# Kernel optimization log

Measured on AMD Instinct MI355X. Metric: run time of the kernel, lower is better.

Reference implementation:

```python
import jax, jax.numpy as jnp
import numpy as np

EMB = 1024
NEG_INF = float(-2**32 + 1)
EPS_SCALE = 1e-8   # epsilon added to sqrt(scale) in attention_dot
LN_EPS = 1e-5      # torch.nn.LayerNorm default eps


def _layernorm(x, w, b):
    mu = jnp.mean(x, axis=-1, keepdims=True)
    var = jnp.mean(jnp.square(x - mu), axis=-1, keepdims=True)
    return (x - mu) * jax.lax.rsqrt(var + LN_EPS) * w + b


def setup_inputs() -> dict:
    key = jax.random.key(0)
    ks = jax.random.split(key, 6)
    B, Lq, Lk, E = 8, 2048, 2048, EMB
    queries = jax.random.normal(ks[0], (B, Lq, E), dtype=jnp.float32)
    keys = jax.random.normal(ks[1], (B, Lk, E), dtype=jnp.float32)
    query_masks = jnp.ones((B, Lq), dtype=jnp.float32)
    key_masks = jnp.ones((B, Lk), dtype=jnp.float32)
    # xavier_uniform for Linear(E, E): limit = sqrt(6/(E+E))
    lim = float(np.sqrt(6.0 / (E + E)))
    W1 = jax.random.uniform(ks[2], (E, E), minval=-lim, maxval=lim, dtype=jnp.float32)
    b1 = jnp.zeros((E,), dtype=jnp.float32)
    W2 = jax.random.uniform(ks[3], (E, E), minval=-lim, maxval=lim, dtype=jnp.float32)
    b2 = jnp.zeros((E,), dtype=jnp.float32)
    ln_w = jnp.ones((E,), dtype=jnp.float32)
    ln_b = jnp.zeros((E,), dtype=jnp.float32)
    ln2_w = jnp.ones((E,), dtype=jnp.float32)
    ln2_b = jnp.zeros((E,), dtype=jnp.float32)
    return {"queries": queries, "keys": keys, "query_masks": query_masks,
            "key_masks": key_masks, "ln_w": ln_w, "ln_b": ln_b,
            "ln2_w": ln2_w, "ln2_b": ln2_b, "W1": W1, "b1": b1,
            "W2": W2, "b2": b2}


def reference(queries, keys, query_masks, key_masks, ln_w, ln_b, ln2_w, ln2_b, W1, b1, W2, b2):
    E = queries.shape[-1]
    # scores [B, Lq, Lk]
    sim = jnp.einsum('bik,bjk->bij', queries, keys)
    sim = sim / (jnp.sqrt(jnp.float32(max(1.0, E))) + EPS_SCALE)
    # key mask applied pre-softmax
    sim = jnp.where(key_masks[:, None, :] == 0, jnp.float32(NEG_INF), sim)
    sim = jax.nn.softmax(sim, axis=-1)
    # query mask applied post-softmax
    sim = sim * query_masks[:, :, None]
    attn_out = jnp.einsum('bij,bjk->bik', sim, keys)
    # residual + LayerNorm
    x = _layernorm(attn_out + queries, ln_w, ln_b)
    # FFN: Linear -> ReLU -> Linear, residual, LayerNorm
    h = jax.nn.relu(x @ W1.T + b1)
    y = h @ W2.T + b2
    return _layernorm(y + x, ln2_w, ln2_b)
```

## Files before the change

### kernel.cpp

```cpp
#include <hip/hip_runtime.h>
#include <hip/hip_bf16.h>
#include <stdint.h>

#define NB    8
#define LQ    2048
#define LKK   2048
#define EMBD  1024

typedef __bf16 bf16_t;
typedef __bf16 bf16x8 __attribute__((ext_vector_type(8)));
typedef __bf16 bf16x4 __attribute__((ext_vector_type(4)));
typedef float  f32x4  __attribute__((ext_vector_type(4)));

__device__ __forceinline__ bf16_t f2bf(float x) {
  union { float f; uint32_t u; } v; v.f = x;
  uint32_t r = v.u + 0x7fffu + ((v.u >> 16) & 1u);
  uint16_t h = (uint16_t)(r >> 16);
  return __builtin_bit_cast(bf16_t, h);
}

__device__ __forceinline__ float wred_sum(float v) {
#pragma unroll
  for (int o = 32; o; o >>= 1) v += __shfl_xor(v, o);
  return v;
}
__device__ __forceinline__ float wred_max(float v) {
#pragma unroll
  for (int o = 32; o; o >>= 1) v = fmaxf(v, __shfl_xor(v, o));
  return v;
}

template<int EPI>
__global__ __launch_bounds__(512, 1)
void gemm_nt(const bf16_t* __restrict__ A, const bf16_t* __restrict__ B,
             float* __restrict__ Cf, bf16_t* __restrict__ Cb,
             const float* __restrict__ bias, float scale,
             int M, int N, int K, long sA, long sB, long sC)
{
  __shared__ __align__(16) char smem[131072];
  typedef bf16_t ldsbuf_t[8][256][8];
  ldsbuf_t* Abuf = (ldsbuf_t*)smem;
  ldsbuf_t* Bbuf = (ldsbuf_t*)(smem + 65536);

  const int tid  = threadIdx.x;
  const int lane = tid & 63;
  const int wave = tid >> 6;
  const int wq   = wave & 3;
  const int bz   = blockIdx.z;

  const bf16_t* Ab = A + (long)bz * sA;
  const bf16_t* Bb = B + (long)bz * sB;

  const int bm = blockIdx.x * 256;
  const int bn = blockIdx.y * 256;
  const int wm = (wave >> 2) * 128;

  f32x4 acc[8][4] = {};

  const int srow = tid & 255;
  const int sslc = tid >> 8;

  const int fr = lane & 15;
  const int fs = lane >> 4;

  auto STAGE = [&](int bufi, int kt) {
#pragma unroll
    for (int i = 0; i < 4; i++) {
      const int slc = sslc + 2 * i;
      __builtin_amdgcn_global_load_lds(
        (const __attribute__((address_space(1))) void*)(Ab + (long)(bm + srow) * K + kt + slc * 8),
        (__attribute__((address_space(3))) void*)((char*)&Abuf[bufi][0][0][0] + (tid + i * 512) * 16),
        16, 0, 0);
    }
#pragma unroll
    for (int i = 0; i < 4; i++) {
      const int slc = sslc + 2 * i;
      __builtin_amdgcn_global_load_lds(
        (const __attribute__((address_space(1))) void*)(Bb + (long)(bn + srow) * K + kt + slc * 8),
        (__attribute__((address_space(3))) void*)((char*)&Bbuf[bufi][0][0][0] + (tid + i * 512) * 16),
        16, 0, 0);
    }
  };

  auto COMPUTE = [&](int bufi) {
#pragma unroll
    for (int kk = 0; kk < 2; kk++) {
      bf16x8 af[8], bfg[4];
#pragma unroll
      for (int m = 0; m < 8; m++)
        af[m] = *(const bf16x8*)&Abuf[bufi][4 * kk + fs][wm + m * 16 + fr][0];
#pragma unroll
      for (int n = 0; n < 4; n++)
        bfg[n] = *(const bf16x8*)&Bbuf[bufi][4 * kk + fs][n * 64 + wq * 16 + fr][0];
#pragma unroll
      for (int m = 0; m < 8; m++)
#pragma unroll
        for (int n = 0; n < 4; n++)
          acc[m][n] = __builtin_amdgcn_mfma_f32_16x16x32_bf16(af[m], bfg[n], acc[m][n], 0, 0, 0);
    }
  };

  STAGE(0, 0);
  __syncthreads();
  int buf = 0;
  for (int kt = 64; kt < K; kt += 64) {
    STAGE(buf ^ 1, kt);
    COMPUTE(buf);
    __syncthreads();
    buf ^= 1;
  }
  COMPUTE(buf);

  float* slab = (float*)smem;
  const long cbase = (long)bz * sC;
#pragma unroll
  for (int h = 0; h < 2; h++) {
    __syncthreads();
#pragma unroll
    for (int nn = 0; nn < 2; nn++) {
      const int n = 2 * h + nn;
      const int colb = nn * 64 + wq * 16 + fr;
#pragma unroll
      for (int m = 0; m < 8; m++) {
        const int rbase = wm + m * 16 + ((lane >> 4) << 2);
#pragma unroll
        for (int j = 0; j < 4; j++) {
          const int row = rbase + j;
          slab[row * 128 + (colb ^ (((row >> 2) & 1) << 4))] = acc[m][n][j];
        }
      }
    }
    __syncthreads();
    const int hcol = bn + h * 128;
    if constexpr (EPI == 3) {
#pragma unroll
      for (int p = 0; p < 16; p++) {
        const int row = p * 16 + (tid >> 5);
        const int c4  = (tid & 31) * 4;
        f32x4 v = *(const f32x4*)&slab[row * 128 + (c4 ^ (((row >> 2) & 1) << 4))];
        const float4 bv = *(const float4*)&bias[hcol + c4];
        v[0] += bv.x; v[1] += bv.y; v[2] += bv.z; v[3] += bv.w;
        *(f32x4*)&Cf[cbase + (long)(bm + row) * N + hcol + c4] = v;
      }
    } else {
#pragma unroll
      for (int p = 0; p < 8; p++) {
        const int row  = p * 32 + (tid >> 4);
        const int c8   = (tid & 15) * 8;
        const int flip = ((row >> 2) & 1) << 4;
        const f32x4 v0 = *(const f32x4*)&slab[row * 128 + (c8 ^ flip)];
        const f32x4 v1 = *(const f32x4*)&slab[row * 128 + ((c8 + 4) ^ flip)];
        const float vv[8] = {v0[0], v0[1], v0[2], v0[3], v1[0], v1[1], v1[2], v1[3]};
        bf16x8 o;
        if constexpr (EPI == 0) {
#pragma unroll
          for (int e = 0; e < 8; e++) o[e] = f2bf(vv[e] * scale);
        } else if constexpr (EPI == 1) {
#pragma unroll
          for (int e = 0; e < 8; e++) o[e] = f2bf(vv[e]);
        } else {
          const float4 b0 = *(const float4*)&bias[hcol + c8];
          const float4 b1 = *(const float4*)&bias[hcol + c8 + 4];
          const float bb[8] = {b0.x, b0.y, b0.z, b0.w, b1.x, b1.y, b1.z, b1.w};
#pragma unroll
          for (int e = 0; e < 8; e++) o[e] = f2bf(fmaxf(vv[e] + bb[e], 0.0f));
        }
        *(bf16x8*)&Cb[cbase + (long)(bm + row) * N + hcol + c8] = o;
      }
    }
  }
}

__global__ __launch_bounds__(256)
void softmax_kernel(const bf16_t* __restrict__ S, bf16_t* __restrict__ P,
                    const float* __restrict__ km, const float* __restrict__ qm)
{
  __shared__ float red[8];
  const int r = blockIdx.x;
  const int b = r >> 11;
  const int t = threadIdx.x;
  const bf16_t* row = S + (long)r * LKK;

  const bf16x8 sv = *(const bf16x8*)(row + t * 8);
  const float4 k0 = ((const float4*)(km + (long)b * LKK))[2 * t];
  const float4 k1 = ((const float4*)(km + (long)b * LKK))[2 * t + 1];
  const float kmv[8] = {k0.x, k0.y, k0.z, k0.w, k1.x, k1.y, k1.z, k1.w};

  float v[8];
  float mx = -3.4e38f;
#pragma unroll
  for (int i = 0; i < 8; i++) {
    float s = (float)sv[i];
    s = (kmv[i] == 0.0f) ? -4294967295.0f : s;
    v[i] = s;
    mx = fmaxf(mx, s);
  }
  mx = wred_max(mx);
  if ((t & 63) == 0) red[t >> 6] = mx;
  __syncthreads();
  mx = fmaxf(fmaxf(red[0], red[1]), fmaxf(red[2], red[3]));

  float sum = 0.0f;
#pragma unroll
  for (int i = 0; i < 8; i++) {
    const float e = __expf(v[i] - mx);
    v[i] = e;
    sum += e;
  }
  sum = wred_sum(sum);
  if ((t & 63) == 0) red[4 + (t >> 6)] = sum;
  __syncthreads();
  sum = red[4] + red[5] + red[6] + red[7];

  const float rs = qm[r] / sum;
  bf16x8 o;
#pragma unroll
  for (int i = 0; i < 8; i++) o[i] = f2bf(v[i] * rs);
  *(bf16x8*)(P + (long)r * LKK + t * 8) = o;
}

template<int MODE>
__global__ __launch_bounds__(256)
void ln_kernel(const void* __restrict__ Xv, const void* __restrict__ Rv,
               const float* __restrict__ w, const float* __restrict__ bp,
               void* __restrict__ Yv)
{
  __shared__ float red[8];
  const long r = blockIdx.x;
  const int t = threadIdx.x;

  float x0, x1, x2, x3;
  if constexpr (MODE & 1) {
    const bf16x4 xv = ((const bf16x4*)((const bf16_t*)Xv + r * EMBD))[t];
    x0 = (float)xv[0]; x1 = (float)xv[1]; x2 = (float)xv[2]; x3 = (float)xv[3];
  } else {
    const float4 xv = ((const float4*)((const float*)Xv + r * EMBD))[t];
    x0 = xv.x; x1 = xv.y; x2 = xv.z; x3 = xv.w;
  }
  float r0, r1, r2, r3;
  if constexpr (MODE & 2) {
    const bf16x4 rv = ((const bf16x4*)((const bf16_t*)Rv + r * EMBD))[t];
    r0 = (float)rv[0]; r1 = (float)rv[1]; r2 = (float)rv[2]; r3 = (float)rv[3];
  } else {
    const float4 rv = ((const float4*)((const float*)Rv + r * EMBD))[t];
    r0 = rv.x; r1 = rv.y; r2 = rv.z; r3 = rv.w;
  }
  const float s0 = x0 + r0, s1 = x1 + r1, s2 = x2 + r2, s3 = x3 + r3;

  float sum = wred_sum(s0 + s1 + s2 + s3);
  if ((t & 63) == 0) red[t >> 6] = sum;
  __syncthreads();
  const float mu = (red[0] + red[1] + red[2] + red[3]) * (1.0f / EMBD);

  const float d0 = s0 - mu, d1 = s1 - mu, d2 = s2 - mu, d3 = s3 - mu;
  float sq = wred_sum(d0 * d0 + d1 * d1 + d2 * d2 + d3 * d3);
  if ((t & 63) == 0) red[4 + (t >> 6)] = sq;
  __syncthreads();
  const float var = (red[4] + red[5] + red[6] + red[7]) * (1.0f / EMBD);
  const float rstd = rsqrtf(var + 1e-5f);

  const float4 wv = ((const float4*)w)[t];
  const float4 bv = ((const float4*)bp)[t];
  const float y0 = d0 * rstd * wv.x + bv.x;
  const float y1 = d1 * rstd * wv.y + bv.y;
  const float y2 = d2 * rstd * wv.z + bv.z;
  const float y3 = d3 * rstd * wv.w + bv.w;

  if constexpr (MODE & 4) {
    bf16x4 o; o[0] = f2bf(y0); o[1] = f2bf(y1); o[2] = f2bf(y2); o[3] = f2bf(y3);
    ((bf16x4*)((bf16_t*)Yv + r * EMBD))[t] = o;
  } else {
    ((float4*)((float*)Yv + r * EMBD))[t] = make_float4(y0, y1, y2, y3);
  }
}

__global__ void cvt_kernel(const float* __restrict__ in, bf16_t* __restrict__ out, long n4)
{
  long i = (long)blockIdx.x * 256 + threadIdx.x;
  const long stride = (long)gridDim.x * 256;
  for (; i < n4; i += stride) {
    const float4 v = ((const float4*)in)[i];
    bf16x4 o; o[0] = f2bf(v.x); o[1] = f2bf(v.y); o[2] = f2bf(v.z); o[3] = f2bf(v.w);
    ((bf16x4*)out)[i] = o;
  }
}

__global__ __launch_bounds__(256)
void transpose_cvt(const float* __restrict__ in, bf16_t* __restrict__ outT,
                   bf16_t* __restrict__ outS, int rows, int cols)
{
  __shared__ bf16_t tile[32][33];
  const long zb = (long)blockIdx.z * rows * cols;
  const int cb = blockIdx.x * 32;
  const int rb = blockIdx.y * 32;
  const int tx = threadIdx.x & 31;
  const int ty = threadIdx.x >> 5;
#pragma unroll
  for (int i = 0; i < 4; i++) {
    const int rr = ty + i * 8;
    const bf16_t v = f2bf(in[zb + (long)(rb + rr) * cols + cb + tx]);
    tile[rr][tx] = v;
    if (outS != nullptr) outS[zb + (long)(rb + rr) * cols + cb + tx] = v;
  }
  __syncthreads();
#pragma unroll
  for (int i = 0; i < 4; i++) {
    const int cc = ty + i * 8;
    outT[zb + (long)(cb + cc) * rows + rb + tx] = tile[tx][cc];
  }
}

extern "C" void kernel_launch(void* const* d_in, const int* in_sizes, int n_in,
                              void* d_out, int out_size, void* d_ws, size_t ws_size,
                              hipStream_t stream)
{
  const float* q    = (const float*)d_in[0];
  const float* k    = (const float*)d_in[1];
  const float* qm   = (const float*)d_in[2];
  const float* km   = (const float*)d_in[3];
  const float* lnw  = (const float*)d_in[4];
  const float* lnb  = (const float*)d_in[5];
  const float* ln2w = (const float*)d_in[6];
  const float* ln2b = (const float*)d_in[7];
  const float* W1   = (const float*)d_in[8];
  const float* b1   = (const float*)d_in[9];
  const float* W2   = (const float*)d_in[10];
  const float* b2   = (const float*)d_in[11];

  char* ws = (char*)d_ws;
  char* ob = (char*)d_out;
  const float scale = 0.03125f;
  const long MB = 1L << 20;
  const long QE = (long)LQ * EMBD;
  const long SS = (long)LQ * LKK;

  if (ws_size >= 100 * MB) {
    bf16_t* Qb   = (bf16_t*)ws;
    bf16_t* attn = (bf16_t*)ws;
    bf16_t* Kb   = (bf16_t*)(ws + 32 * MB);
    bf16_t* h    = (bf16_t*)(ws + 32 * MB);
    bf16_t* Kt   = (bf16_t*)(ws + 64 * MB);
    bf16_t* W1b  = (bf16_t*)(ws + 96 * MB);
    bf16_t* W2b  = (bf16_t*)(ws + 98 * MB);
    bf16_t* Sb   = (bf16_t*)ob;
    float*  y    = (float*)ob;

    cvt_kernel<<<1024, 256, 0, stream>>>(W1, W1b, (long)EMBD * EMBD / 4);
    cvt_kernel<<<1024, 256, 0, stream>>>(W2, W2b, (long)EMBD * EMBD / 4);
    cvt_kernel<<<4096, 256, 0, stream>>>(q, Qb, (long)NB * QE / 4);
    transpose_cvt<<<dim3(EMBD / 32, LKK / 32, NB), 256, 0, stream>>>(k, Kt, Kb, LKK, EMBD);

    gemm_nt<0><<<dim3(LQ / 256, LKK / 256, NB), 512, 0, stream>>>(
        Qb, Kb, nullptr, Sb, nullptr, scale, LQ, LKK, EMBD, QE, QE, SS);
    softmax_kernel<<<NB * LQ, 256, 0, stream>>>(Sb, Sb, km, qm);
    gemm_nt<1><<<dim3(LQ / 256, EMBD / 256, NB), 512, 0, stream>>>(
        Sb, Kt, nullptr, attn, nullptr, 0.0f, LQ, EMBD, LKK, SS, (long)EMBD * LKK, QE);
    ln_kernel<5><<<NB * LQ, 256, 0, stream>>>(attn, q, lnw, lnb, attn);
    gemm_nt<2><<<dim3(NB * LQ / 256, EMBD / 256, 1), 512, 0, stream>>>(
        attn, W1b, nullptr, h, b1, 0.0f, NB * LQ, EMBD, EMBD, 0, 0, 0);
    gemm_nt<3><<<dim3(NB * LQ / 256, EMBD / 256, 1), 512, 0, stream>>>(
        h, W2b, y, nullptr, b2, 0.0f, NB * LQ, EMBD, EMBD, 0, 0, 0);
    ln_kernel<2><<<NB * LQ, 256, 0, stream>>>(y, attn, ln2w, ln2b, y);

  } else if (ws_size >= 52 * MB) {
    bf16_t* attn = (bf16_t*)ws;
    bf16_t* W1b  = (bf16_t*)(ws + 32 * MB);
    bf16_t* W2b  = (bf16_t*)(ws + 34 * MB);
    bf16_t* Kth  = (bf16_t*)(ws + 36 * MB);
    bf16_t* h    = (bf16_t*)(ws + 36 * MB);
    bf16_t* Sb   = (bf16_t*)ob;
    bf16_t* Qbh  = (bf16_t*)(ob + 32 * MB);
    bf16_t* Kbh  = (bf16_t*)(ob + 48 * MB);
    float*  y    = (float*)ob;

    cvt_kernel<<<1024, 256, 0, stream>>>(W1, W1b, (long)EMBD * EMBD / 4);
    cvt_kernel<<<1024, 256, 0, stream>>>(W2, W2b, (long)EMBD * EMBD / 4);

    for (int it = 0; it < 2; it++) {
      const int bo = it * 4;
      const float* qh = q + bo * QE;
      const float* kh = k + bo * QE;
      cvt_kernel<<<2048, 256, 0, stream>>>(qh, Qbh, 4 * QE / 4);
      transpose_cvt<<<dim3(EMBD / 32, LKK / 32, 4), 256, 0, stream>>>(kh, Kth, Kbh, LKK, EMBD);

      gemm_nt<0><<<dim3(LQ / 256, LKK / 256, 4), 512, 0, stream>>>(
          Qbh, Kbh, nullptr, Sb, nullptr, scale, LQ, LKK, EMBD, QE, QE, SS);
      softmax_kernel<<<4 * LQ, 256, 0, stream>>>(Sb, Sb, km + bo * LKK, qm + bo * LQ);
      gemm_nt<1><<<dim3(LQ / 256, EMBD / 256, 4), 512, 0, stream>>>(
          Sb, Kth, nullptr, attn + bo * QE, nullptr, 0.0f, LQ, EMBD, LKK,
          SS, (long)EMBD * LKK, QE);
    }
    ln_kernel<5><<<NB * LQ, 256, 0, stream>>>(attn, q, lnw, lnb, attn);
    for (int c = 0; c < 2; c++) {
      bf16_t* xc = attn + (long)c * 8192 * EMBD;
      float*  yc = y + (long)c * 8192 * EMBD;
      gemm_nt<2><<<dim3(8192 / 256, EMBD / 256, 1), 512, 0, stream>>>(
          xc, W1b, nullptr, h, b1, 0.0f, 8192, EMBD, EMBD, 0, 0, 0);
      gemm_nt<3><<<dim3(8192 / 256, EMBD / 256, 1), 512, 0, stream>>>(
          h, W2b, yc, nullptr, b2, 0.0f, 8192, EMBD, EMBD, 0, 0, 0);
    }
    ln_kernel<2><<<NB * LQ, 256, 0, stream>>>(y, attn, ln2w, ln2b, y);

  } else {
    if (ws_size < 44 * MB) return;
    bf16_t* attn = (bf16_t*)ws;
    bf16_t* W1b  = (bf16_t*)(ws + 32 * MB);
    bf16_t* W2b  = (bf16_t*)(ws + 34 * MB);
    bf16_t* h    = (bf16_t*)(ws + 36 * MB);
    bf16_t* Sb   = (bf16_t*)(ob);
    bf16_t* Pb   = (bf16_t*)(ob + 8 * MB);
    bf16_t* Qbb  = (bf16_t*)(ob + 16 * MB);
    bf16_t* Kbb  = (bf16_t*)(ob + 20 * MB);
    bf16_t* Ktb  = (bf16_t*)(ob + 24 * MB);

    cvt_kernel<<<1024, 256, 0, stream>>>(W1, W1b, (long)EMBD * EMBD / 4);
    cvt_kernel<<<1024, 256, 0, stream>>>(W2, W2b, (long)EMBD * EMBD / 4);

    for (int b = 0; b < NB; b++) {
      const float* qb = q + b * QE;
      const float* kb = k + b * QE;
      cvt_kernel<<<2048, 256, 0, stream>>>(qb, Qbb, QE / 4);
      transpose_cvt<<<dim3(EMBD / 32, LKK / 32, 1), 256, 0, stream>>>(kb, Ktb, Kbb, LKK, EMBD);

      gemm_nt<0><<<dim3(LQ / 256, LKK / 256, 1), 512, 0, stream>>>(
          Qbb, Kbb, nullptr, Sb, nullptr, scale, LQ, LKK, EMBD, 0, 0, 0);
      softmax_kernel<<<LQ, 256, 0, stream>>>(Sb, Pb, km + (long)b * LKK, qm + (long)b * LQ);
      gemm_nt<1><<<dim3(LQ / 256, EMBD / 256, 1), 512, 0, stream>>>(
          Pb, Ktb, nullptr, attn + b * QE, nullptr, 0.0f, LQ, EMBD, LKK, 0, 0, 0);
    }
    ln_kernel<5><<<NB * LQ, 256, 0, stream>>>(attn, q, lnw, lnb, attn);
    for (int c = 0; c < 4; c++) {
      bf16_t* xc = attn + (long)c * 4096 * EMBD;
      float*  yc = (float*)d_out + (long)c * 4096 * EMBD;
      gemm_nt<2><<<dim3(4096 / 256, EMBD / 256, 1), 512, 0, stream>>>(
          xc, W1b, nullptr, h, b1, 0.0f, 4096, EMBD, EMBD, 0, 0, 0);
      gemm_nt<3><<<dim3(4096 / 256, EMBD / 256, 1), 512, 0, stream>>>(
          h, W2b, yc, nullptr, b2, 0.0f, 4096, EMBD, EMBD, 0, 0, 0);
      ln_kernel<2><<<4096, 256, 0, stream>>>(yc, xc, ln2w, ln2b, yc);
    }
  }
}
```

Baseline: 456.0 us.

## Add 32-wide K GEMM variant with 64KB LDS for two blocks per CU

Adds gemm_nt32, which stages K in steps of 32 instead of 64, halving LDS to 64KB and declaring launch bounds of two blocks per CU. The intent is higher occupancy, so one block's memory stalls can overlap with another's MFMA work. The epilogue is factored out and now writes the slab in four 64-column passes with a new XOR swizzle, so it fits in the smaller LDS. The QK, PV and first FFN GEMMs switch to the new kernel. The risks are twice as many barriers per K, and register pressure from the 128-float accumulator when capped for two blocks, which could cause spills.

```diff
diff --git a/kernel.cpp b/kernel.cpp
--- a/kernel.cpp
+++ b/kernel.cpp
@@ -28,6 +28,72 @@
 #pragma unroll
   for (int o = 32; o; o >>= 1) v = fmaxf(v, __shfl_xor(v, o));
   return v;
+}
+
+__device__ __forceinline__ int slab_flip(int row) {
+  return ((row ^ (row >> 2)) & 3) << 4;
+}
+
+template<int EPI>
+__device__ __forceinline__ void gemm_epilogue(
+    f32x4 (&acc)[8][4], char* smem, float* Cf, bf16_t* Cb,
+    const float* bias, float scale, int N, long cbase,
+    int bm, int bn, int wm, int wq, int tid, int lane)
+{
+  float* slab = (float*)smem;
+  const int fr = lane & 15;
+  const int g4 = (lane >> 4) << 2;
+#pragma unroll
+  for (int n = 0; n < 4; n++) {
+    __syncthreads();
+#pragma unroll
+    for (int m = 0; m < 8; m++) {
+      const int rbase = wm + m * 16 + g4;
+#pragma unroll
+      for (int j = 0; j < 4; j++) {
+        const int row = rbase + j;
+        slab[row * 64 + ((wq * 16 + fr) ^ slab_flip(row))] = acc[m][n][j];
+      }
+    }
+    __syncthreads();
+    const int ncol = bn + n * 64;
+    if constexpr (EPI == 3) {
+#pragma unroll
+      for (int p = 0; p < 8; p++) {
+        const int row = p * 32 + (tid >> 4);
+        const int c4  = (tid & 15) * 4;
+        f32x4 v = *(const f32x4*)&slab[row * 64 + (c4 ^ slab_flip(row))];
+        const float4 bv = *(const float4*)&bias[ncol + c4];
+        v[0] += bv.x; v[1] += bv.y; v[2] += bv.z; v[3] += bv.w;
+        *(f32x4*)&Cf[cbase + (long)(bm + row) * N + ncol + c4] = v;
+      }
+    } else {
+#pragma unroll
+      for (int p = 0; p < 4; p++) {
+        const int row  = p * 64 + (tid >> 3);
+        const int c8   = (tid & 7) * 8;
+        const int flip = slab_flip(row);
+        const f32x4 v0 = *(const f32x4*)&slab[row * 64 + (c8 ^ flip)];
+        const f32x4 v1 = *(const f32x4*)&slab[row * 64 + ((c8 + 4) ^ flip)];
+        const float vv[8] = {v0[0], v0[1], v0[2], v0[3], v1[0], v1[1], v1[2], v1[3]};
+        bf16x8 o;
+        if constexpr (EPI == 0) {
+#pragma unroll
+          for (int e = 0; e < 8; e++) o[e] = f2bf(vv[e] * scale);
+        } else if constexpr (EPI == 1) {
+#pragma unroll
+          for (int e = 0; e < 8; e++) o[e] = f2bf(vv[e]);
+        } else {
+          const float4 b0 = *(const float4*)&bias[ncol + c8];
+          const float4 b1 = *(const float4*)&bias[ncol + c8 + 4];
+          const float bb[8] = {b0.x, b0.y, b0.z, b0.w, b1.x, b1.y, b1.z, b1.w};
+#pragma unroll
+          for (int e = 0; e < 8; e++) o[e] = f2bf(fmaxf(vv[e] + bb[e], 0.0f));
+        }
+        *(bf16x8*)&Cb[cbase + (long)(bm + row) * N + ncol + c8] = o;
+      }
+    }
+  }
 }
 
 template<int EPI>
@@ -111,64 +177,86 @@
   }
   COMPUTE(buf);
 
-  float* slab = (float*)smem;
-  const long cbase = (long)bz * sC;
-#pragma unroll
-  for (int h = 0; h < 2; h++) {
+  gemm_epilogue<EPI>(acc, smem, Cf, Cb, bias, scale, N, (long)bz * sC,
+                     bm, bn, wm, wq, tid, lane);
+}
+
+template<int EPI>
+__global__ __launch_bounds__(512, 2)
+void gemm_nt32(const bf16_t* __restrict__ A, const bf16_t* __restrict__ B,
+               float* __restrict__ Cf, bf16_t* __restrict__ Cb,
+               const float* __restrict__ bias, float scale,
+               int M, int N, int K, long sA, long sB, long sC)
+{
+  __shared__ __align__(16) char smem[65536];
+  typedef bf16_t ldsbuf_t[4][256][8];
+  ldsbuf_t* Abuf = (ldsbuf_t*)smem;
+  ldsbuf_t* Bbuf = (ldsbuf_t*)(smem + 32768);
+
+  const int tid  = threadIdx.x;
+  const int lane = tid & 63;
+  const int wave = tid >> 6;
+  const int wq   = wave & 3;
+  const int bz   = blockIdx.z;
+
+  const bf16_t* Ab = A + (long)bz * sA;
+  const bf16_t* Bb = B + (long)bz * sB;
+
+  const int bm = blockIdx.x * 256;
+  const int bn = blockIdx.y * 256;
+  const int wm = (wave >> 2) * 128;
+
+  f32x4 acc[8][4] = {};
+
+  const int srow = tid & 255;
+  const int sslc = tid >> 8;
+
+  const int fr = lane & 15;
+  const int fs = lane >> 4;
+
+  auto STAGE = [&](int bufi, int kt) {
+#pragma unroll
+    for (int i = 0; i < 2; i++) {
+      const int slc = sslc + 2 * i;
+      __builtin_amdgcn_global_load_lds(
+        (const __attribute__((address_space(1))) void*)(Ab + (long)(bm + srow) * K + kt + slc * 8),
+        (__attribute__((address_space(3))) void*)((char*)&Abuf[bufi][0][0][0] + (tid + i * 512) * 16),
+        16, 0, 0);
+      __builtin_amdgcn_global_load_lds(
+        (const __attribute__((address_space(1))) void*)(Bb + (long)(bn + srow) * K + kt + slc * 8),
+        (__attribute__((address_space(3))) void*)((char*)&Bbuf[bufi][0][0][0] + (tid + i * 512) * 16),
+        16, 0, 0);
+    }
+  };
+
+  auto COMPUTE = [&](int bufi) {
+    bf16x8 af[8], bfg[4];
+#pragma unroll
+    for (int m = 0; m < 8; m++)
+      af[m] = *(const bf16x8*)&Abuf[bufi][fs][wm + m * 16 + fr][0];
+#pragma unroll
+    for (int n = 0; n < 4; n++)
+      bfg[n] = *(const bf16x8*)&Bbuf[bufi][fs][n * 64 + wq * 16 + fr][0];
+#pragma unroll
+    for (int m = 0; m < 8; m++)
+#pragma unroll
+      for (int n = 0; n < 4; n++)
+        acc[m][n] = __builtin_amdgcn_mfma_f32_16x16x32_bf16(af[m], bfg[n], acc[m][n], 0, 0, 0);
+  };
+
+  STAGE(0, 0);
+  __syncthreads();
+  int buf = 0;
+  for (int kt = 32; kt < K; kt += 32) {
+    STAGE(buf ^ 1, kt);
+    COMPUTE(buf);
     __syncthreads();
-#pragma unroll
-    for (int nn = 0; nn < 2; nn++) {
-      const int n = 2 * h + nn;
-      const int colb = nn * 64 + wq * 16 + fr;
-#pragma unroll
-      for (int m = 0; m < 8; m++) {
-        const int rbase = wm + m * 16 + ((lane >> 4) << 2);
-#pragma unroll
-        for (int j = 0; j < 4; j++) {
-          const int row = rbase + j;
-          slab[row * 128 + (colb ^ (((row >> 2) & 1) << 4))] = acc[m][n][j];
-        }
-      }
-    }
-    __syncthreads();
-    const int hcol = bn + h * 128;
-    if constexpr (EPI == 3) {
-#pragma unroll
-      for (int p = 0; p < 16; p++) {
-        const int row = p * 16 + (tid >> 5);
-        const int c4  = (tid & 31) * 4;
-        f32x4 v = *(const f32x4*)&slab[row * 128 + (c4 ^ (((row >> 2) & 1) << 4))];
-        const float4 bv = *(const float4*)&bias[hcol + c4];
-        v[0] += bv.x; v[1] += bv.y; v[2] += bv.z; v[3] += bv.w;
-        *(f32x4*)&Cf[cbase + (long)(bm + row) * N + hcol + c4] = v;
-      }
-    } else {
-#pragma unroll
-      for (int p = 0; p < 8; p++) {
-        const int row  = p * 32 + (tid >> 4);
-        const int c8   = (tid & 15) * 8;
-        const int flip = ((row >> 2) & 1) << 4;
-        const f32x4 v0 = *(const f32x4*)&slab[row * 128 + (c8 ^ flip)];
-        const f32x4 v1 = *(const f32x4*)&slab[row * 128 + ((c8 + 4) ^ flip)];
-        const float vv[8] = {v0[0], v0[1], v0[2], v0[3], v1[0], v1[1], v1[2], v1[3]};
-        bf16x8 o;
-        if constexpr (EPI == 0) {
-#pragma unroll
-          for (int e = 0; e < 8; e++) o[e] = f2bf(vv[e] * scale);
-        } else if constexpr (EPI == 1) {
-#pragma unroll
-          for (int e = 0; e < 8; e++) o[e] = f2bf(vv[e]);
-        } else {
-          const float4 b0 = *(const float4*)&bias[hcol + c8];
-          const float4 b1 = *(const float4*)&bias[hcol + c8 + 4];
-          const float bb[8] = {b0.x, b0.y, b0.z, b0.w, b1.x, b1.y, b1.z, b1.w};
-#pragma unroll
-          for (int e = 0; e < 8; e++) o[e] = f2bf(fmaxf(vv[e] + bb[e], 0.0f));
-        }
-        *(bf16x8*)&Cb[cbase + (long)(bm + row) * N + hcol + c8] = o;
-      }
-    }
-  }
+    buf ^= 1;
+  }
+  COMPUTE(buf);
+
+  gemm_epilogue<EPI>(acc, smem, Cf, Cb, bias, scale, N, (long)bz * sC,
+                     bm, bn, wm, wq, tid, lane);
 }
 
 __global__ __launch_bounds__(256)
@@ -350,13 +438,13 @@
     cvt_kernel<<<4096, 256, 0, stream>>>(q, Qb, (long)NB * QE / 4);
     transpose_cvt<<<dim3(EMBD / 32, LKK / 32, NB), 256, 0, stream>>>(k, Kt, Kb, LKK, EMBD);
 
-    gemm_nt<0><<<dim3(LQ / 256, LKK / 256, NB), 512, 0, stream>>>(
+    gemm_nt32<0><<<dim3(LQ / 256, LKK / 256, NB), 512, 0, stream>>>(
         Qb, Kb, nullptr, Sb, nullptr, scale, LQ, LKK, EMBD, QE, QE, SS);
     softmax_kernel<<<NB * LQ, 256, 0, stream>>>(Sb, Sb, km, qm);
-    gemm_nt<1><<<dim3(LQ / 256, EMBD / 256, NB), 512, 0, stream>>>(
+    gemm_nt32<1><<<dim3(LQ / 256, EMBD / 256, NB), 512, 0, stream>>>(
         Sb, Kt, nullptr, attn, nullptr, 0.0f, LQ, EMBD, LKK, SS, (long)EMBD * LKK, QE);
     ln_kernel<5><<<NB * LQ, 256, 0, stream>>>(attn, q, lnw, lnb, attn);
-    gemm_nt<2><<<dim3(NB * LQ / 256, EMBD / 256, 1), 512, 0, stream>>>(
+    gemm_nt32<2><<<dim3(NB * LQ / 256, EMBD / 256, 1), 512, 0, stream>>>(
         attn, W1b, nullptr, h, b1, 0.0f, NB * LQ, EMBD, EMBD, 0, 0, 0);
     gemm_nt<3><<<dim3(NB * LQ / 256, EMBD / 256, 1), 512, 0, stream>>>(
         h, W2b, y, nullptr, b2, 0.0f, NB * LQ, EMBD, EMBD, 0, 0, 0);
@@ -383,10 +471,10 @@
       cvt_kernel<<<2048, 256, 0, stream>>>(qh, Qbh, 4 * QE / 4);
       transpose_cvt<<<dim3(EMBD / 32, LKK / 32, 4), 256, 0, stream>>>(kh, Kth, Kbh, LKK, EMBD);
 
-      gemm_nt<0><<<dim3(LQ / 256, LKK / 256, 4), 512, 0, stream>>>(
+      gemm_nt32<0><<<dim3(LQ / 256, LKK / 256, 4), 512, 0, stream>>>(
           Qbh, Kbh, nullptr, Sb, nullptr, scale, LQ, LKK, EMBD, QE, QE, SS);
       softmax_kernel<<<4 * LQ, 256, 0, stream>>>(Sb, Sb, km + bo * LKK, qm + bo * LQ);
-      gemm_nt<1><<<dim3(LQ / 256, EMBD / 256, 4), 512, 0, stream>>>(
+      gemm_nt32<1><<<dim3(LQ / 256, EMBD / 256, 4), 512, 0, stream>>>(
           Sb, Kth, nullptr, attn + bo * QE, nullptr, 0.0f, LQ, EMBD, LKK,
           SS, (long)EMBD * LKK, QE);
     }
@@ -394,7 +482,7 @@
     for (int c = 0; c < 2; c++) {
       bf16_t* xc = attn + (long)c * 8192 * EMBD;
       float*  yc = y + (long)c * 8192 * EMBD;
-      gemm_nt<2><<<dim3(8192 / 256, EMBD / 256, 1), 512, 0, stream>>>(
+      gemm_nt32<2><<<dim3(8192 / 256, EMBD / 256, 1), 512, 0, stream>>>(
           xc, W1b, nullptr, h, b1, 0.0f, 8192, EMBD, EMBD, 0, 0, 0);
       gemm_nt<3><<<dim3(8192 / 256, EMBD / 256, 1), 512, 0, stream>>>(
           h, W2b, yc, nullptr, b2, 0.0f, 8192, EMBD, EMBD, 0, 0, 0);
@@ -422,17 +510,17 @@
       cvt_kernel<<<2048, 256, 0, stream>>>(qb, Qbb, QE / 4);
       transpose_cvt<<<dim3(EMBD / 32, LKK / 32, 1), 256, 0, stream>>>(kb, Ktb, Kbb, LKK, EMBD);
 
-      gemm_nt<0><<<dim3(LQ / 256, LKK / 256, 1), 512, 0, stream>>>(
+      gemm_nt32<0><<<dim3(LQ / 256, LKK / 256, 1), 512, 0, stream>>>(
           Qbb, Kbb, nullptr, Sb, nullptr, scale, LQ, LKK, EMBD, 0, 0, 0);
       softmax_kernel<<<LQ, 256, 0, stream>>>(Sb, Pb, km + (long)b * LKK, qm + (long)b * LQ);
-      gemm_nt<1><<<dim3(LQ / 256, EMBD / 256, 1), 512, 0, stream>>>(
+      gemm_nt32<1><<<dim3(LQ / 256, EMBD / 256, 1), 512, 0, stream>>>(
           Pb, Ktb, nullptr, attn + b * QE, nullptr, 0.0f, LQ, EMBD, LKK, 0, 0, 0);
     }
     ln_kernel<5><<<NB * LQ, 256, 0, stream>>>(attn, q, lnw, lnb, attn);
     for (int c = 0; c < 4; c++) {
       bf16_t* xc = attn + (long)c * 4096 * EMBD;
       float*  yc = (float*)d_out + (long)c * 4096 * EMBD;
-      gemm_nt<2><<<dim3(4096 / 256, EMBD / 256, 1), 512, 0, stream>>>(
+      gemm_nt32<2><<<dim3(4096 / 256, EMBD / 256, 1), 512, 0, stream>>>(
           xc, W1b, nullptr, h, b1, 0.0f, 4096, EMBD, EMBD, 0, 0, 0);
       gemm_nt<3><<<dim3(4096 / 256, EMBD / 256, 1), 512, 0, stream>>>(
           h, W2b, yc, nullptr, b2, 0.0f, 4096, EMBD, EMBD, 0, 0, 0);
```

Measured after the change: 581.9 us. 1.28x slower.

## Add finely interleaved 8-wave GEMM pipeline for the P·K attention matmul

Applied to the files above, without the earlier changes.

Pulls the GEMM epilogue out into a shared device function and adds a new gemm_nt8 kernel. It splits each 64-wide K tile's global-to-LDS staging into four chunks, interleaved with four MFMA phases under explicit barriers, waitcnts and s_setprio. Only the second (P·K) GEMM uses it. The aim is to hide load latency behind matrix math and let MFMA-issuing waves take priority, at the cost of many more barriers per tile and hand-tuned vmcnt counts that must match the staging order.

```diff
diff --git a/kernel.cpp b/kernel.cpp
--- a/kernel.cpp
+++ b/kernel.cpp
@@ -31,88 +31,13 @@
 }
 
 template<int EPI>
-__global__ __launch_bounds__(512, 1)
-void gemm_nt(const bf16_t* __restrict__ A, const bf16_t* __restrict__ B,
-             float* __restrict__ Cf, bf16_t* __restrict__ Cb,
-             const float* __restrict__ bias, float scale,
-             int M, int N, int K, long sA, long sB, long sC)
-{
-  __shared__ __align__(16) char smem[131072];
-  typedef bf16_t ldsbuf_t[8][256][8];
-  ldsbuf_t* Abuf = (ldsbuf_t*)smem;
-  ldsbuf_t* Bbuf = (ldsbuf_t*)(smem + 65536);
-
-  const int tid  = threadIdx.x;
-  const int lane = tid & 63;
-  const int wave = tid >> 6;
-  const int wq   = wave & 3;
-  const int bz   = blockIdx.z;
-
-  const bf16_t* Ab = A + (long)bz * sA;
-  const bf16_t* Bb = B + (long)bz * sB;
-
-  const int bm = blockIdx.x * 256;
-  const int bn = blockIdx.y * 256;
-  const int wm = (wave >> 2) * 128;
-
-  f32x4 acc[8][4] = {};
-
-  const int srow = tid & 255;
-  const int sslc = tid >> 8;
-
+__device__ __forceinline__ void gemm_epilogue(
+    f32x4 (&acc)[8][4], char* smem, float* Cf, bf16_t* Cb,
+    const float* bias, float scale, int N, long cbase,
+    int bm, int bn, int wm, int wq, int tid, int lane)
+{
+  float* slab = (float*)smem;
   const int fr = lane & 15;
-  const int fs = lane >> 4;
-
-  auto STAGE = [&](int bufi, int kt) {
-#pragma unroll
-    for (int i = 0; i < 4; i++) {
-      const int slc = sslc + 2 * i;
-      __builtin_amdgcn_global_load_lds(
-        (const __attribute__((address_space(1))) void*)(Ab + (long)(bm + srow) * K + kt + slc * 8),
-        (__attribute__((address_space(3))) void*)((char*)&Abuf[bufi][0][0][0] + (tid + i * 512) * 16),
-        16, 0, 0);
-    }
-#pragma unroll
-    for (int i = 0; i < 4; i++) {
-      const int slc = sslc + 2 * i;
-      __builtin_amdgcn_global_load_lds(
-        (const __attribute__((address_space(1))) void*)(Bb + (long)(bn + srow) * K + kt + slc * 8),
-        (__attribute__((address_space(3))) void*)((char*)&Bbuf[bufi][0][0][0] + (tid + i * 512) * 16),
-        16, 0, 0);
-    }
-  };
-
-  auto COMPUTE = [&](int bufi) {
-#pragma unroll
-    for (int kk = 0; kk < 2; kk++) {
-      bf16x8 af[8], bfg[4];
-#pragma unroll
-      for (int m = 0; m < 8; m++)
-        af[m] = *(const bf16x8*)&Abuf[bufi][4 * kk + fs][wm + m * 16 + fr][0];
-#pragma unroll
-      for (int n = 0; n < 4; n++)
-        bfg[n] = *(const bf16x8*)&Bbuf[bufi][4 * kk + fs][n * 64 + wq * 16 + fr][0];
-#pragma unroll
-      for (int m = 0; m < 8; m++)
-#pragma unroll
-        for (int n = 0; n < 4; n++)
-          acc[m][n] = __builtin_amdgcn_mfma_f32_16x16x32_bf16(af[m], bfg[n], acc[m][n], 0, 0, 0);
-    }
-  };
-
-  STAGE(0, 0);
-  __syncthreads();
-  int buf = 0;
-  for (int kt = 64; kt < K; kt += 64) {
-    STAGE(buf ^ 1, kt);
-    COMPUTE(buf);
-    __syncthreads();
-    buf ^= 1;
-  }
-  COMPUTE(buf);
-
-  float* slab = (float*)smem;
-  const long cbase = (long)bz * sC;
 #pragma unroll
   for (int h = 0; h < 2; h++) {
     __syncthreads();
@@ -169,6 +94,206 @@
       }
     }
   }
+}
+
+template<int EPI>
+__global__ __launch_bounds__(512, 1)
+void gemm_nt(const bf16_t* __restrict__ A, const bf16_t* __restrict__ B,
+             float* __restrict__ Cf, bf16_t* __restrict__ Cb,
+             const float* __restrict__ bias, float scale,
+             int M, int N, int K, long sA, long sB, long sC)
+{
+  __shared__ __align__(16) char smem[131072];
+  typedef bf16_t ldsbuf_t[8][256][8];
+  ldsbuf_t* Abuf = (ldsbuf_t*)smem;
+  ldsbuf_t* Bbuf = (ldsbuf_t*)(smem + 65536);
+
+  const int tid  = threadIdx.x;
+  const int lane = tid & 63;
+  const int wave = tid >> 6;
+  const int wq   = wave & 3;
+  const int bz   = blockIdx.z;
+
+  const bf16_t* Ab = A + (long)bz * sA;
+  const bf16_t* Bb = B + (long)bz * sB;
+
+  const int bm = blockIdx.x * 256;
+  const int bn = blockIdx.y * 256;
+  const int wm = (wave >> 2) * 128;
+
+  f32x4 acc[8][4] = {};
+
+  const int srow = tid & 255;
+  const int sslc = tid >> 8;
+
+  const int fr = lane & 15;
+  const int fs = lane >> 4;
+
+  auto STAGE = [&](int bufi, int kt) {
+#pragma unroll
+    for (int i = 0; i < 4; i++) {
+      const int slc = sslc + 2 * i;
+      __builtin_amdgcn_global_load_lds(
+        (const __attribute__((address_space(1))) void*)(Ab + (long)(bm + srow) * K + kt + slc * 8),
+        (__attribute__((address_space(3))) void*)((char*)&Abuf[bufi][0][0][0] + (tid + i * 512) * 16),
+        16, 0, 0);
+    }
+#pragma unroll
+    for (int i = 0; i < 4; i++) {
+      const int slc = sslc + 2 * i;
+      __builtin_amdgcn_global_load_lds(
+        (const __attribute__((address_space(1))) void*)(Bb + (long)(bn + srow) * K + kt + slc * 8),
+        (__attribute__((address_space(3))) void*)((char*)&Bbuf[bufi][0][0][0] + (tid + i * 512) * 16),
+        16, 0, 0);
+    }
+  };
+
+  auto COMPUTE = [&](int bufi) {
+#pragma unroll
+    for (int kk = 0; kk < 2; kk++) {
+      bf16x8 af[8], bfg[4];
+#pragma unroll
+      for (int m = 0; m < 8; m++)
+        af[m] = *(const bf16x8*)&Abuf[bufi][4 * kk + fs][wm + m * 16 + fr][0];
+#pragma unroll
+      for (int n = 0; n < 4; n++)
+        bfg[n] = *(const bf16x8*)&Bbuf[bufi][4 * kk + fs][n * 64 + wq * 16 + fr][0];
+#pragma unroll
+      for (int m = 0; m < 8; m++)
+#pragma unroll
+        for (int n = 0; n < 4; n++)
+          acc[m][n] = __builtin_amdgcn_mfma_f32_16x16x32_bf16(af[m], bfg[n], acc[m][n], 0, 0, 0);
+    }
+  };
+
+  STAGE(0, 0);
+  __syncthreads();
+  int buf = 0;
+  for (int kt = 64; kt < K; kt += 64) {
+    STAGE(buf ^ 1, kt);
+    COMPUTE(buf);
+    __syncthreads();
+    buf ^= 1;
+  }
+  COMPUTE(buf);
+
+  gemm_epilogue<EPI>(acc, smem, Cf, Cb, bias, scale, N, (long)bz * sC,
+                     bm, bn, wm, wq, tid, lane);
+}
+
+template<int EPI>
+__global__ __launch_bounds__(512, 1)
+void gemm_nt8(const bf16_t* __restrict__ A, const bf16_t* __restrict__ B,
+              float* __restrict__ Cf, bf16_t* __restrict__ Cb,
+              const float* __restrict__ bias, float scale,
+              int M, int N, int K, long sA, long sB, long sC)
+{
+  __shared__ __align__(16) char smem[131072];
+  typedef bf16_t ldsbuf_t[8][256][8];
+  ldsbuf_t* Abuf = (ldsbuf_t*)smem;
+  ldsbuf_t* Bbuf = (ldsbuf_t*)(smem + 65536);
+
+  const int tid  = threadIdx.x;
+  const int lane = tid & 63;
+  const int wave = tid >> 6;
+  const int wq   = wave & 3;
+  const int bz   = blockIdx.z;
+
+  const bf16_t* Ab = A + (long)bz * sA;
+  const bf16_t* Bb = B + (long)bz * sB;
+
+  const int bm = blockIdx.x * 256;
+  const int bn = blockIdx.y * 256;
+  const int wm = (wave >> 2) * 128;
+
+  f32x4 acc[8][4] = {};
+
+  const int fr = lane & 15;
+  const int fs = lane >> 4;
+
+  auto STAGE_CHUNK = [&](int bufi, int kt, int c) {
+    const bf16_t* src = (c & 1) ? Bb : Ab;
+    const int base    = (c & 1) ? bn : bm;
+    char* dst = ((c & 1) ? (char*)&Bbuf[bufi][0][0][0] : (char*)&Abuf[bufi][0][0][0])
+                + (c >> 1) * 16384;
+    const int kofs = kt + (c >> 1) * 32;
+#pragma unroll
+    for (int i = 0; i < 2; i++) {
+      const int slot = tid + i * 512;
+      const int slc  = slot >> 8;
+      const int row  = slot & 255;
+      __builtin_amdgcn_global_load_lds(
+        (const __attribute__((address_space(1))) void*)(src + (long)(base + row) * K + kofs + slc * 8),
+        (__attribute__((address_space(3))) void*)(dst + slot * 16), 16, 0, 0);
+    }
+  };
+
+  auto MFMA16 = [&](bf16x8 (&af)[8], bf16x8 bx, bf16x8 by, int n0, int n1) {
+    __builtin_amdgcn_s_setprio(1);
+#pragma unroll
+    for (int m = 0; m < 8; m++)
+      acc[m][n0] = __builtin_amdgcn_mfma_f32_16x16x32_bf16(af[m], bx, acc[m][n0], 0, 0, 0);
+#pragma unroll
+    for (int m = 0; m < 8; m++)
+      acc[m][n1] = __builtin_amdgcn_mfma_f32_16x16x32_bf16(af[m], by, acc[m][n1], 0, 0, 0);
+    __builtin_amdgcn_s_setprio(0);
+  };
+
+  const int nt = K >> 6;
+
+  STAGE_CHUNK(0, 0, 0); STAGE_CHUNK(0, 0, 1);
+  STAGE_CHUNK(0, 0, 2); STAGE_CHUNK(0, 0, 3);
+  asm volatile("s_waitcnt vmcnt(4)" ::: "memory");
+  __builtin_amdgcn_s_barrier();
+
+  for (int t = 0; t < nt; ++t) {
+    const int cur = t & 1, nxt = cur ^ 1;
+    const bool pf = (t + 1 < nt);
+    const int ktn = (t + 1) << 6;
+    bf16x8 af[8], b0, b1;
+
+#pragma unroll
+    for (int m = 0; m < 8; m++) af[m] = *(const bf16x8*)&Abuf[cur][fs][wm + m * 16 + fr][0];
+    b0 = *(const bf16x8*)&Bbuf[cur][fs][wq * 16 + fr][0];
+    b1 = *(const bf16x8*)&Bbuf[cur][fs][64 + wq * 16 + fr][0];
+    if (pf) STAGE_CHUNK(nxt, ktn, 0);
+    __builtin_amdgcn_s_barrier();
+    asm volatile("s_waitcnt lgkmcnt(0)" ::: "memory");
+    MFMA16(af, b0, b1, 0, 1);
+    __builtin_amdgcn_s_barrier();
+
+    b0 = *(const bf16x8*)&Bbuf[cur][fs][128 + wq * 16 + fr][0];
+    b1 = *(const bf16x8*)&Bbuf[cur][fs][192 + wq * 16 + fr][0];
+    if (pf) STAGE_CHUNK(nxt, ktn, 1);
+    __builtin_amdgcn_s_barrier();
+    asm volatile("s_waitcnt lgkmcnt(0)" ::: "memory");
+    MFMA16(af, b0, b1, 2, 3);
+    if (pf) asm volatile("s_waitcnt vmcnt(4)" ::: "memory");
+    else    asm volatile("s_waitcnt vmcnt(0)" ::: "memory");
+    __builtin_amdgcn_s_barrier();
+
+#pragma unroll
+    for (int m = 0; m < 8; m++) af[m] = *(const bf16x8*)&Abuf[cur][4 + fs][wm + m * 16 + fr][0];
+    b0 = *(const bf16x8*)&Bbuf[cur][4 + fs][wq * 16 + fr][0];
+    b1 = *(const bf16x8*)&Bbuf[cur][4 + fs][64 + wq * 16 + fr][0];
+    if (pf) STAGE_CHUNK(nxt, ktn, 2);
+    __builtin_amdgcn_s_barrier();
+    asm volatile("s_waitcnt lgkmcnt(0)" ::: "memory");
+    MFMA16(af, b0, b1, 0, 1);
+    __builtin_amdgcn_s_barrier();
+
+    b0 = *(const bf16x8*)&Bbuf[cur][4 + fs][128 + wq * 16 + fr][0];
+    b1 = *(const bf16x8*)&Bbuf[cur][4 + fs][192 + wq * 16 + fr][0];
+    if (pf) STAGE_CHUNK(nxt, ktn, 3);
+    __builtin_amdgcn_s_barrier();
+    asm volatile("s_waitcnt lgkmcnt(0)" ::: "memory");
+    MFMA16(af, b0, b1, 2, 3);
+    if (pf) asm volatile("s_waitcnt vmcnt(4)" ::: "memory");
+    __builtin_amdgcn_s_barrier();
+  }
+
+  gemm_epilogue<EPI>(acc, smem, Cf, Cb, bias, scale, N, (long)bz * sC,
+                     bm, bn, wm, wq, tid, lane);
 }
 
 __global__ __launch_bounds__(256)
@@ -353,7 +478,7 @@
     gemm_nt<0><<<dim3(LQ / 256, LKK / 256, NB), 512, 0, stream>>>(
         Qb, Kb, nullptr, Sb, nullptr, scale, LQ, LKK, EMBD, QE, QE, SS);
     softmax_kernel<<<NB * LQ, 256, 0, stream>>>(Sb, Sb, km, qm);
-    gemm_nt<1><<<dim3(LQ / 256, EMBD / 256, NB), 512, 0, stream>>>(
+    gemm_nt8<1><<<dim3(LQ / 256, EMBD / 256, NB), 512, 0, stream>>>(
         Sb, Kt, nullptr, attn, nullptr, 0.0f, LQ, EMBD, LKK, SS, (long)EMBD * LKK, QE);
     ln_kernel<5><<<NB * LQ, 256, 0, stream>>>(attn, q, lnw, lnb, attn);
     gemm_nt<2><<<dim3(NB * LQ / 256, EMBD / 256, 1), 512, 0, stream>>>(
```

Measured after the change: 447.8 us. No clear change (-1.8%).
